# Optimization experiments

Hardware: AMD Instinct MI355X
Metric: run time of the kernel (lower is better)

Reference implementation:

```python
import jax, jax.numpy as jnp
import numpy as np

EPS = 1e-7  # keras.backend.epsilon()
B, U, F = 1024, 256, 31
D = 1 + U + F  # features dim after concat


def setup_inputs() -> dict:
    key = jax.random.key(0)
    ks = jax.random.split(key, 9)
    s = 1.0 / np.sqrt(D)
    return {
        "last_cell": jax.random.uniform(ks[0], (B, U), dtype=jnp.float32),
        "input_precipitation": jax.random.uniform(ks[1], (B,), dtype=jnp.float32),
        "input_other_features": jax.random.normal(ks[2], (B, F), dtype=jnp.float32),
        "W_i": jax.random.normal(ks[3], (D, U), dtype=jnp.float32) * s,
        "b_i": jnp.zeros((U,), dtype=jnp.float32),
        "W_r": jax.random.normal(ks[4], (D, U * U), dtype=jnp.float32) * s,
        "b_r": jnp.zeros((U * U,), dtype=jnp.float32),
        "W_o": jax.random.normal(ks[5], (D, U), dtype=jnp.float32) * s,
        "b_o": jnp.zeros((U,), dtype=jnp.float32),
    }


def reference(last_cell, input_precipitation, input_other_features,
              W_i, b_i, W_r, b_r, W_o, b_o):
    # L1-normalize last cell state (mass fractions)
    l1 = jnp.sum(jnp.abs(last_cell), axis=-1, keepdims=True) + EPS
    last_cell_hat = last_cell / l1
    p = input_precipitation[:, None]  # [B,1]
    features = jnp.concatenate([p, last_cell_hat, input_other_features], axis=-1)  # [B,D]

    # input gate: sigmoid then L1-normalized across units (mass-conserving split)
    ig = jax.nn.sigmoid(features @ W_i + b_i)
    ig = ig / jnp.sum(jnp.abs(ig), axis=-1, keepdims=True)

    # redistribution matrix: relu, reshape [B,U,U], L1-normalize each row
    R = jax.nn.relu(features @ W_r + b_r).reshape(-1, U, U)
    R = R / jnp.sum(jnp.abs(R), axis=-1, keepdims=True)

    # output gate: sigmoid
    og = jax.nn.sigmoid(features @ W_o + b_o)

    cell_in = ig * p                                   # [B,U]
    cell_sys = jnp.einsum('bu,buv->bv', last_cell, R)  # batched (1xU)@(UxU)
    candidate = cell_in + cell_sys
    output = og * candidate
    cell = (1.0 - og) * candidate
    return (cell, output)
```

## Files before the change

### kernel.cpp

```cpp
#include <hip/hip_runtime.h>


#define EPS_L1 1e-7f

constexpr int BB  = 1024;
constexpr int U   = 256;
constexpr int F   = 31;
constexpr int D   = 1 + U + F;
constexpr int NBV = BB * U;
constexpr int NCH = D / 32;
constexpr int UIMGB = NCH * 16384;
constexpr size_t WTB_BYTES  = (size_t)258 * UIMGB;
constexpr size_t FEAT_BYTES = (size_t)BB * D * 2;
constexpr int PITCH = 260;

typedef float f32x4 __attribute__((ext_vector_type(4)));
typedef short bf16x8 __attribute__((ext_vector_type(8)));

__device__ __forceinline__ unsigned f2bf(float x) {
  union { float f; unsigned u; } v; v.f = x;
  unsigned r = v.u + 0x7FFFu + ((v.u >> 16) & 1u);
  return r >> 16;
}

#define GLDS16(gp, lp)                                                        \
  __builtin_amdgcn_global_load_lds(                                          \
      (const __attribute__((address_space(1))) void*)(gp),                   \
      (__attribute__((address_space(3))) void*)(lp), 16, 0, 0)

#define MFMA16(a, b, c) __builtin_amdgcn_mfma_f32_16x16x32_bf16((a), (b), (c), 0, 0, 0)

__global__ __launch_bounds__(256) void k_prepW(
    const float* __restrict__ Wi, const float* __restrict__ Wr,
    const float* __restrict__ Wo, short* __restrict__ WtB) {
  __shared__ short lds[2][32 * PITCH];
  const int bid = blockIdx.x, t = threadIdx.x;
  const int u = bid / 3, part = bid % 3;
  const float* src; long ld;
  if (u < 256)       { src = Wr + (size_t)u * 256; ld = 65536; }
  else if (u == 256) { src = Wi; ld = 256; }
  else               { src = Wo; ld = 256; }
  short* dst = WtB + (size_t)u * 73728;
  const int lane = t & 63, wave = t >> 6;
  const int g = lane >> 4, l15 = lane & 15;

#pragma unroll
  for (int cc = 0; cc < 3; ++cc) {
    const int c = part * 3 + cc;
    short* buf = lds[cc & 1];
#pragma unroll
    for (int i = 0; i < 8; ++i) {
      const int f = i * 256 + t;
      const int row = f >> 6, col4 = f & 63;
      const float4 v = *(const float4*)(src + (size_t)(c * 32 + row) * ld + col4 * 4);
      const unsigned lo = f2bf(v.x) | (f2bf(v.y) << 16);
      const unsigned hi = f2bf(v.z) | (f2bf(v.w) << 16);
      unsigned* wp = (unsigned*)&buf[row * PITCH + col4 * 4];
      wp[0] = lo; wp[1] = hi;
    }
    __syncthreads();
#pragma unroll
    for (int i = 0; i < 4; ++i) {
      const int n0 = wave * 4 + i;
      bf16x8 h;
#pragma unroll
      for (int j = 0; j < 8; ++j)
        h[j] = buf[(g * 8 + j) * PITCH + n0 * 16 + l15];
      *(bf16x8*)(dst + (size_t)(c * 16 + n0) * 512 + lane * 8) = h;
    }
    __syncthreads();
  }
}

__global__ __launch_bounds__(256) void k_prepF(
    const float* __restrict__ lc, const float* __restrict__ p,
    const float* __restrict__ other, short* __restrict__ featImg,
    float* __restrict__ cell_sys) {
  __shared__ float inv_s[64];
  const int bid = blockIdx.x, t = threadIdx.x;
  if (bid < 16) {
    const int b0 = bid * 64;
    const int row = t >> 2, q = t & 3;
    const float4* lp = (const float4*)(lc + (size_t)(b0 + row) * 256 + q * 64);
    float s = 0.f;
#pragma unroll
    for (int j = 0; j < 16; ++j) {
      const float4 v = lp[j];
      s += fabsf(v.x) + fabsf(v.y) + fabsf(v.z) + fabsf(v.w);
    }
    s += __shfl_xor(s, 1, 64);
    s += __shfl_xor(s, 2, 64);
    if (q == 0) inv_s[row] = 1.f / (s + EPS_L1);
    __syncthreads();
#pragma unroll
    for (int i = 0; i < 9; ++i) {
      const int idx = i * 256 + t;
      const int reg = idx >> 6, l = idx & 63;
      const int c = reg >> 2, mt = reg & 3;
      const int lrow = mt * 16 + (l & 15);
      const int grow = b0 + lrow;
      const int k0 = c * 32 + (l >> 4) * 8;
      bf16x8 h;
#pragma unroll
      for (int j = 0; j < 8; ++j) {
        const int k = k0 + j;
        float v;
        if (k == 0) v = p[grow];
        else if (k <= 256) v = lc[(size_t)grow * 256 + (k - 1)] * inv_s[lrow];
        else v = other[(size_t)grow * 31 + (k - 257)];
        h[j] = (short)f2bf(v);
      }
      *(bf16x8*)(featImg + (size_t)bid * 18432 + (size_t)reg * 512 + l * 8) = h;
    }
  } else {
    float4* cs4 = (float4*)cell_sys;
    const int base = (bid - 16) * 8192 + t;
    const float4 z = {0.f, 0.f, 0.f, 0.f};
#pragma unroll
    for (int k2 = 0; k2 < 32; ++k2) cs4[base + k2 * 256] = z;
  }
}

__global__ __launch_bounds__(256, 2) void k_heavyR6(
    const short* __restrict__ featImg, const short* __restrict__ WtB,
    const float* __restrict__ lc, const float* __restrict__ br,
    float* __restrict__ cell_sys) {
  __shared__ short aT[18432];
  __shared__ float rsum[2][64][4];
  __shared__ float lcs[2][64];

  const int t = threadIdx.x, lane = t & 63, cq = t >> 6;
  const int quad = lane >> 4, l15 = lane & 15;
  const int bid = blockIdx.x;
  const int Mb = (bid >> 3) & 15;
  const int ug = (bid & 7) * 4 + (bid >> 7);
  const int b0 = Mb * 64, u0 = ug * 8;

  {
    const char* gA = (const char*)featImg + (size_t)Mb * 36864;
    char* lA = (char*)aT;
#pragma unroll
    for (int i = 0; i < 9; ++i)
      GLDS16(gA + i * 4096 + t * 16, lA + i * 4096 + t * 16);
  }

  const char* aB = (const char*)aT + lane * 16;
  const char* bB = (const char*)WtB + (size_t)u0 * UIMGB + cq * 4096 + lane * 16;

  f32x4 acc[4][4], outa[4][4];
#pragma unroll
  for (int m = 0; m < 4; ++m)
#pragma unroll
    for (int n = 0; n < 4; ++n)
#pragma unroll
      for (int r = 0; r < 4; ++r) { acc[m][n][r] = 0.f; outa[m][n][r] = 0.f; }

  bf16x8 bfr[3][4];
#pragma unroll
  for (int n = 0; n < 4; ++n) bfr[0][n] = *(const bf16x8*)(bB + n * 1024);
#pragma unroll
  for (int n = 0; n < 4; ++n) bfr[1][n] = *(const bf16x8*)(bB + 16384 + n * 1024);

  __syncthreads();

  bf16x8 afr[2][4];
#pragma unroll
  for (int m = 0; m < 4; ++m) afr[0][m] = *(const bf16x8*)(aB + m * 1024);

  for (int uu = 0; uu < 8; ++uu) {
    const int u = u0 + uu;
    float bv[4];
#pragma unroll
    for (int n = 0; n < 4; ++n)
      bv[n] = br[(size_t)u * 256 + cq * 64 + n * 16 + l15];
    if (t < 64) lcs[uu & 1][t] = lc[(size_t)(b0 + t) * 256 + u];

#pragma unroll
    for (int c = 0; c < 9; ++c) {
#pragma unroll
      for (int n = 0; n < 4; ++n)
        bfr[(c + 2) % 3][n] = *(const bf16x8*)(bB + (c + 2) * 16384 + n * 1024);
      if (c < 8) {
#pragma unroll
        for (int m = 0; m < 4; ++m)
          afr[(c + 1) & 1][m] = *(const bf16x8*)(aB + (c + 1) * 4096 + m * 1024);
      }
#pragma unroll
      for (int m = 0; m < 4; ++m)
#pragma unroll
        for (int n = 0; n < 4; ++n)
          acc[m][n] = MFMA16(afr[c & 1][m], bfr[c % 3][n], acc[m][n]);
    }
    bB += UIMGB;

#pragma unroll
    for (int m = 0; m < 4; ++m) afr[0][m] = *(const bf16x8*)(aB + m * 1024);

    const int ub = uu & 1;
    float sm[4][4];
#pragma unroll
    for (int m = 0; m < 4; ++m)
#pragma unroll
      for (int r = 0; r < 4; ++r) {
        float sv = 0.f;
#pragma unroll
        for (int n = 0; n < 4; ++n) {
          const float rv = fmaxf(acc[m][n][r] + bv[n], 0.f);
          acc[m][n][r] = rv;
          sv += rv;
        }
        sm[m][r] = sv;
      }
#pragma unroll
    for (int msk = 1; msk < 16; msk <<= 1)
#pragma unroll
      for (int m = 0; m < 4; ++m)
#pragma unroll
        for (int r = 0; r < 4; ++r)
          sm[m][r] += __shfl_xor(sm[m][r], msk, 64);
    if (l15 == 0) {
#pragma unroll
      for (int m = 0; m < 4; ++m)
#pragma unroll
        for (int r = 0; r < 4; ++r)
          rsum[ub][m * 16 + quad * 4 + r][cq] = sm[m][r];
    }
    __syncthreads();
#pragma unroll
    for (int m = 0; m < 4; ++m)
#pragma unroll
      for (int r = 0; r < 4; ++r) {
        const int row = m * 16 + quad * 4 + r;
        const float4 rv = *(const float4*)&rsum[ub][row][0];
        const float tot = (rv.x + rv.y) + (rv.z + rv.w);
        const float alpha = lcs[ub][row] * __builtin_amdgcn_rcpf(tot);
#pragma unroll
        for (int n = 0; n < 4; ++n) {
          outa[m][n][r] = fmaf(alpha, acc[m][n][r], outa[m][n][r]);
          acc[m][n][r] = 0.f;
        }
      }
  }

#pragma unroll
  for (int m = 0; m < 4; ++m)
#pragma unroll
    for (int r = 0; r < 4; ++r) {
      const int grow = b0 + m * 16 + quad * 4 + r;
#pragma unroll
      for (int n = 0; n < 4; ++n)
        atomicAdd(&cell_sys[(size_t)grow * 256 + cq * 64 + n * 16 + l15],
                  outa[m][n][r]);
    }
}

__global__ __launch_bounds__(512, 2) void k_post(
    const short* __restrict__ featImg, const short* __restrict__ WtB,
    const float* __restrict__ bi, const float* __restrict__ bo,
    const float* __restrict__ p, const float* __restrict__ cell_sys,
    float* __restrict__ dout) {
  __shared__ short aT[18432];
  __shared__ float rsum[64][12];
  __shared__ float ps[64];

  const int t = threadIdx.x, lane = t & 63, cg = t >> 6;
  const int quad = lane >> 4, l15 = lane & 15;
  const int mb = blockIdx.x, b0 = mb * 64;

  {
    const char* gsrc = (const char*)featImg + (size_t)mb * 36864;
    char* lbase = (char*)aT;
#pragma unroll
    for (int i = 0; i < 5; ++i) {
      if (i * 8 + cg < 36) {
        const int off = i * 8192 + t * 16;
        GLDS16(gsrc + off, lbase + off);
      }
    }
  }
  if (t < 64) ps[t] = p[b0 + t];

  f32x4 acc[4][2];
#pragma unroll
  for (int mt = 0; mt < 4; ++mt)
#pragma unroll
    for (int n = 0; n < 2; ++n)
#pragma unroll
      for (int r = 0; r < 4; ++r) acc[mt][n][r] = 0.f;

  const char* bptr = (const char*)WtB + (size_t)256 * UIMGB + cg * 2048 + lane * 16;
  bf16x8 cb0 = *(const bf16x8*)(bptr);
  bf16x8 cb1 = *(const bf16x8*)(bptr + 1024);
  bf16x8 nb0 = *(const bf16x8*)(bptr + 16384);
  bf16x8 nb1 = *(const bf16x8*)(bptr + 16384 + 1024);
  bptr += 32768;

  __syncthreads();

  float ig0[4][4], ig1[4][4], og0[4][4], og1[4][4];

#pragma unroll
  for (int g = 0; g < 2; ++g) {
    const float* bias = (g == 0) ? bi : bo;
    const float bv0 = bias[cg * 32 + l15];
    const float bv1 = bias[cg * 32 + 16 + l15];
#pragma unroll
    for (int c = 0; c < 9; ++c) {
      const bf16x8 pb0 = *(const bf16x8*)(bptr);
      const bf16x8 pb1 = *(const bf16x8*)(bptr + 1024);
      bptr += 16384;
      const char* ab = (const char*)aT + c * 4096 + lane * 16;
      const bf16x8 a0 = *(const bf16x8*)(ab);
      const bf16x8 a1 = *(const bf16x8*)(ab + 1024);
      const bf16x8 a2 = *(const bf16x8*)(ab + 2048);
      const bf16x8 a3 = *(const bf16x8*)(ab + 3072);
      acc[0][0] = MFMA16(a0, cb0, acc[0][0]);
      acc[0][1] = MFMA16(a0, cb1, acc[0][1]);
      acc[1][0] = MFMA16(a1, cb0, acc[1][0]);
      acc[1][1] = MFMA16(a1, cb1, acc[1][1]);
      acc[2][0] = MFMA16(a2, cb0, acc[2][0]);
      acc[2][1] = MFMA16(a2, cb1, acc[2][1]);
      acc[3][0] = MFMA16(a3, cb0, acc[3][0]);
      acc[3][1] = MFMA16(a3, cb1, acc[3][1]);
      cb0 = nb0; cb1 = nb1; nb0 = pb0; nb1 = pb1;
    }

#pragma unroll
    for (int mt = 0; mt < 4; ++mt)
#pragma unroll
      for (int r = 0; r < 4; ++r) {
        const float v0 = 1.f / (1.f + __expf(-(acc[mt][0][r] + bv0)));
        const float v1 = 1.f / (1.f + __expf(-(acc[mt][1][r] + bv1)));
        if (g == 0) { ig0[mt][r] = v0; ig1[mt][r] = v1; }
        else        { og0[mt][r] = v0; og1[mt][r] = v1; }
        acc[mt][0][r] = 0.f;
        acc[mt][1][r] = 0.f;
      }

    if (g == 0) {
      float sm[4][4];
#pragma unroll
      for (int mt = 0; mt < 4; ++mt)
#pragma unroll
        for (int r = 0; r < 4; ++r) sm[mt][r] = ig0[mt][r] + ig1[mt][r];
#pragma unroll
      for (int msk = 1; msk < 16; msk <<= 1)
#pragma unroll
        for (int mt = 0; mt < 4; ++mt)
#pragma unroll
          for (int r = 0; r < 4; ++r)
            sm[mt][r] += __shfl_xor(sm[mt][r], msk, 64);
      if (l15 == 0) {
#pragma unroll
        for (int mt = 0; mt < 4; ++mt)
#pragma unroll
          for (int r = 0; r < 4; ++r)
            rsum[mt * 16 + quad * 4 + r][cg] = sm[mt][r];
      }
      __syncthreads();
#pragma unroll
      for (int mt = 0; mt < 4; ++mt)
#pragma unroll
        for (int r = 0; r < 4; ++r) {
          const int row = mt * 16 + quad * 4 + r;
          const float4 ra = *(const float4*)&rsum[row][0];
          const float4 rb = *(const float4*)&rsum[row][4];
          const float inv = 1.f / (((ra.x + ra.y) + (ra.z + ra.w)) +
                                   ((rb.x + rb.y) + (rb.z + rb.w)));
          ig0[mt][r] *= inv;
          ig1[mt][r] *= inv;
        }
    }
  }

#pragma unroll
  for (int mt = 0; mt < 4; ++mt)
#pragma unroll
    for (int r = 0; r < 4; ++r) {
      const int row = mt * 16 + quad * 4 + r;
      const float pr = ps[row];
      const size_t base = (size_t)(b0 + row) * 256 + cg * 32 + l15;
      {
        const float cand = fmaf(ig0[mt][r], pr, cell_sys[base]);
        dout[base] = (1.f - og0[mt][r]) * cand;
        dout[NBV + base] = og0[mt][r] * cand;
      }
      {
        const float cand = fmaf(ig1[mt][r], pr, cell_sys[base + 16]);
        dout[base + 16] = (1.f - og1[mt][r]) * cand;
        dout[NBV + base + 16] = og1[mt][r] * cand;
      }
    }
}

extern "C" void kernel_launch(void* const* d_in, const int* in_sizes, int n_in,
                              void* d_out, int out_size, void* d_ws, size_t ws_size,
                              hipStream_t stream) {
  const float* lc    = (const float*)d_in[0];
  const float* p     = (const float*)d_in[1];
  const float* other = (const float*)d_in[2];
  const float* Wi    = (const float*)d_in[3];
  const float* bi    = (const float*)d_in[4];
  const float* Wr    = (const float*)d_in[5];
  const float* br    = (const float*)d_in[6];
  const float* Wo    = (const float*)d_in[7];
  const float* bo    = (const float*)d_in[8];
  float* out = (float*)d_out;

  char* wsb = (char*)d_ws;
  short* WtB      = (short*)wsb;
  short* featImg  = (short*)(wsb + WTB_BYTES);
  float* cell_sys = (float*)(wsb + WTB_BYTES + FEAT_BYTES);

  k_prepW<<<774, 256, 0, stream>>>(Wi, Wr, Wo, WtB);
  k_prepF<<<24, 256, 0, stream>>>(lc, p, other, featImg, cell_sys);
  k_heavyR6<<<512, 256, 0, stream>>>(featImg, WtB, lc, br, cell_sys);
  k_post<<<16, 512, 0, stream>>>(featImg, WtB, bi, bo, p, cell_sys, out);
}
```

Baseline: 222.8 us.

## Switch to 32x32 MFMA, fold gate GEMMs into heavy kernel, add final elementwise pass

Re-lays out the bf16 weight and feature images for 32x32x16 MFMA tiles and rewrites the heavy redistribution kernel to use them, halving accumulator tile count and cross-lane reduction width changes. The input/output gate GEMMs move from the separate k_post kernel into 16 extra blocks of the heavy kernel that write ig and og to the output buffer, and a new small elementwise kernel combines them with cell_sys. This aims to cut MFMA instruction count and remove the serialized low-occupancy post kernel, at the cost of an extra global round trip for ig/og and an additional launch.

```diff
diff --git a/kernel.cpp b/kernel.cpp
--- a/kernel.cpp
+++ b/kernel.cpp
@@ -14,7 +14,7 @@
 constexpr size_t FEAT_BYTES = (size_t)BB * D * 2;
 constexpr int PITCH = 260;
 
-typedef float f32x4 __attribute__((ext_vector_type(4)));
+typedef float f32x16 __attribute__((ext_vector_type(16)));
 typedef short bf16x8 __attribute__((ext_vector_type(8)));
 
 __device__ __forceinline__ unsigned f2bf(float x) {
@@ -28,7 +28,7 @@
       (const __attribute__((address_space(1))) void*)(gp),                   \
       (__attribute__((address_space(3))) void*)(lp), 16, 0, 0)
 
-#define MFMA16(a, b, c) __builtin_amdgcn_mfma_f32_16x16x32_bf16((a), (b), (c), 0, 0, 0)
+#define MFMA32(a, b, c) __builtin_amdgcn_mfma_f32_32x32x16_bf16((a), (b), (c), 0, 0, 0)
 
 __global__ __launch_bounds__(256) void k_prepW(
     const float* __restrict__ Wi, const float* __restrict__ Wr,
@@ -42,7 +42,7 @@
   else               { src = Wo; ld = 256; }
   short* dst = WtB + (size_t)u * 73728;
   const int lane = t & 63, wave = t >> 6;
-  const int g = lane >> 4, l15 = lane & 15;
+  const int g2 = lane >> 5, l31 = lane & 31;
 
 #pragma unroll
   for (int cc = 0; cc < 3; ++cc) {
@@ -62,11 +62,12 @@
 #pragma unroll
     for (int i = 0; i < 4; ++i) {
       const int n0 = wave * 4 + i;
-      bf16x8 h;
+      const int nt = n0 >> 1, h = n0 & 1;
+      bf16x8 hv;
 #pragma unroll
       for (int j = 0; j < 8; ++j)
-        h[j] = buf[(g * 8 + j) * PITCH + n0 * 16 + l15];
-      *(bf16x8*)(dst + (size_t)(c * 16 + n0) * 512 + lane * 8) = h;
+        hv[j] = buf[(h * 16 + g2 * 8 + j) * PITCH + nt * 32 + l31];
+      *(bf16x8*)(dst + (size_t)(c * 16 + n0) * 512 + lane * 8) = hv;
     }
     __syncthreads();
   }
@@ -96,11 +97,12 @@
     for (int i = 0; i < 9; ++i) {
       const int idx = i * 256 + t;
       const int reg = idx >> 6, l = idx & 63;
-      const int c = reg >> 2, mt = reg & 3;
-      const int lrow = mt * 16 + (l & 15);
+      const int c = reg >> 2, sub = reg & 3;
+      const int mt = sub >> 1, h = sub & 1;
+      const int lrow = mt * 32 + (l & 31);
       const int grow = b0 + lrow;
-      const int k0 = c * 32 + (l >> 4) * 8;
-      bf16x8 h;
+      const int k0 = c * 32 + h * 16 + (l >> 5) * 8;
+      bf16x8 hv;
 #pragma unroll
       for (int j = 0; j < 8; ++j) {
         const int k = k0 + j;
@@ -108,9 +110,9 @@
         if (k == 0) v = p[grow];
         else if (k <= 256) v = lc[(size_t)grow * 256 + (k - 1)] * inv_s[lrow];
         else v = other[(size_t)grow * 31 + (k - 257)];
-        h[j] = (short)f2bf(v);
-      }
-      *(bf16x8*)(featImg + (size_t)bid * 18432 + (size_t)reg * 512 + l * 8) = h;
+        hv[j] = (short)f2bf(v);
+      }
+      *(bf16x8*)(featImg + (size_t)bid * 18432 + (size_t)reg * 512 + l * 8) = hv;
     }
   } else {
     float4* cs4 = (float4*)cell_sys;
@@ -121,20 +123,23 @@
   }
 }
 
-__global__ __launch_bounds__(256, 2) void k_heavyR6(
+__global__ __launch_bounds__(256, 2) void k_heavyG(
     const short* __restrict__ featImg, const short* __restrict__ WtB,
     const float* __restrict__ lc, const float* __restrict__ br,
-    float* __restrict__ cell_sys) {
+    const float* __restrict__ bi, const float* __restrict__ bo,
+    float* __restrict__ cell_sys, float* __restrict__ dout) {
   __shared__ short aT[18432];
   __shared__ float rsum[2][64][4];
   __shared__ float lcs[2][64];
 
   const int t = threadIdx.x, lane = t & 63, cq = t >> 6;
-  const int quad = lane >> 4, l15 = lane & 15;
+  const int g2 = lane >> 5, l31 = lane & 31;
   const int bid = blockIdx.x;
-  const int Mb = (bid >> 3) & 15;
-  const int ug = (bid & 7) * 4 + (bid >> 7);
-  const int b0 = Mb * 64, u0 = ug * 8;
+  const bool is_gate = bid >= 512;
+  const int Mb = is_gate ? (bid - 512) : ((bid >> 3) & 15);
+  const int ug = is_gate ? 0 : ((bid & 7) * 4 + (bid >> 7));
+  const int b0 = Mb * 64;
+  const int u0 = ug * 8;
 
   {
     const char* gA = (const char*)featImg + (size_t)Mb * 36864;
@@ -145,252 +150,221 @@
   }
 
   const char* aB = (const char*)aT + lane * 16;
-  const char* bB = (const char*)WtB + (size_t)u0 * UIMGB + cq * 4096 + lane * 16;
-
-  f32x4 acc[4][4], outa[4][4];
-#pragma unroll
-  for (int m = 0; m < 4; ++m)
-#pragma unroll
-    for (int n = 0; n < 4; ++n)
-#pragma unroll
-      for (int r = 0; r < 4; ++r) { acc[m][n][r] = 0.f; outa[m][n][r] = 0.f; }
+  const char* bB = (const char*)WtB +
+      (is_gate ? (size_t)256 * UIMGB : (size_t)u0 * UIMGB) +
+      cq * 4096 + lane * 16;
+
+  f32x16 acc[2][2];
+#pragma unroll
+  for (int m = 0; m < 2; ++m)
+#pragma unroll
+    for (int n = 0; n < 2; ++n)
+#pragma unroll
+      for (int r = 0; r < 16; ++r) acc[m][n][r] = 0.f;
 
   bf16x8 bfr[3][4];
 #pragma unroll
-  for (int n = 0; n < 4; ++n) bfr[0][n] = *(const bf16x8*)(bB + n * 1024);
-#pragma unroll
-  for (int n = 0; n < 4; ++n) bfr[1][n] = *(const bf16x8*)(bB + 16384 + n * 1024);
+  for (int q = 0; q < 4; ++q) bfr[0][q] = *(const bf16x8*)(bB + q * 1024);
+#pragma unroll
+  for (int q = 0; q < 4; ++q) bfr[1][q] = *(const bf16x8*)(bB + 16384 + q * 1024);
 
   __syncthreads();
 
   bf16x8 afr[2][4];
 #pragma unroll
-  for (int m = 0; m < 4; ++m) afr[0][m] = *(const bf16x8*)(aB + m * 1024);
-
-  for (int uu = 0; uu < 8; ++uu) {
-    const int u = u0 + uu;
-    float bv[4];
-#pragma unroll
-    for (int n = 0; n < 4; ++n)
-      bv[n] = br[(size_t)u * 256 + cq * 64 + n * 16 + l15];
-    if (t < 64) lcs[uu & 1][t] = lc[(size_t)(b0 + t) * 256 + u];
-
-#pragma unroll
-    for (int c = 0; c < 9; ++c) {
-#pragma unroll
-      for (int n = 0; n < 4; ++n)
-        bfr[(c + 2) % 3][n] = *(const bf16x8*)(bB + (c + 2) * 16384 + n * 1024);
-      if (c < 8) {
-#pragma unroll
-        for (int m = 0; m < 4; ++m)
-          afr[(c + 1) & 1][m] = *(const bf16x8*)(aB + (c + 1) * 4096 + m * 1024);
-      }
-#pragma unroll
-      for (int m = 0; m < 4; ++m)
-#pragma unroll
-        for (int n = 0; n < 4; ++n)
-          acc[m][n] = MFMA16(afr[c & 1][m], bfr[c % 3][n], acc[m][n]);
-    }
-    bB += UIMGB;
-
-#pragma unroll
-    for (int m = 0; m < 4; ++m) afr[0][m] = *(const bf16x8*)(aB + m * 1024);
-
-    const int ub = uu & 1;
-    float sm[4][4];
-#pragma unroll
-    for (int m = 0; m < 4; ++m)
-#pragma unroll
-      for (int r = 0; r < 4; ++r) {
-        float sv = 0.f;
-#pragma unroll
-        for (int n = 0; n < 4; ++n) {
-          const float rv = fmaxf(acc[m][n][r] + bv[n], 0.f);
-          acc[m][n][r] = rv;
-          sv += rv;
-        }
-        sm[m][r] = sv;
-      }
-#pragma unroll
-    for (int msk = 1; msk < 16; msk <<= 1)
-#pragma unroll
-      for (int m = 0; m < 4; ++m)
-#pragma unroll
-        for (int r = 0; r < 4; ++r)
-          sm[m][r] += __shfl_xor(sm[m][r], msk, 64);
-    if (l15 == 0) {
-#pragma unroll
-      for (int m = 0; m < 4; ++m)
-#pragma unroll
-        for (int r = 0; r < 4; ++r)
-          rsum[ub][m * 16 + quad * 4 + r][cq] = sm[m][r];
-    }
-    __syncthreads();
-#pragma unroll
-    for (int m = 0; m < 4; ++m)
-#pragma unroll
-      for (int r = 0; r < 4; ++r) {
-        const int row = m * 16 + quad * 4 + r;
-        const float4 rv = *(const float4*)&rsum[ub][row][0];
-        const float tot = (rv.x + rv.y) + (rv.z + rv.w);
-        const float alpha = lcs[ub][row] * __builtin_amdgcn_rcpf(tot);
-#pragma unroll
-        for (int n = 0; n < 4; ++n) {
-          outa[m][n][r] = fmaf(alpha, acc[m][n][r], outa[m][n][r]);
-          acc[m][n][r] = 0.f;
-        }
-      }
+  for (int q = 0; q < 4; ++q) afr[0][q] = *(const bf16x8*)(aB + q * 1024);
+
+  if (!is_gate) {
+    f32x16 outa[2][2];
+#pragma unroll
+    for (int m = 0; m < 2; ++m)
+#pragma unroll
+      for (int n = 0; n < 2; ++n)
+#pragma unroll
+        for (int r = 0; r < 16; ++r) outa[m][n][r] = 0.f;
+
+    for (int uu = 0; uu < 8; ++uu) {
+      const int u = u0 + uu;
+      float bv[2];
+#pragma unroll
+      for (int n = 0; n < 2; ++n)
+        bv[n] = br[(size_t)u * 256 + cq * 64 + n * 32 + l31];
+      if (t < 64) lcs[uu & 1][t] = lc[(size_t)(b0 + t) * 256 + u];
+
+#pragma unroll
+      for (int c = 0; c < 9; ++c) {
+#pragma unroll
+        for (int q = 0; q < 4; ++q)
+          bfr[(c + 2) % 3][q] = *(const bf16x8*)(bB + (c + 2) * 16384 + q * 1024);
+        if (c < 8) {
+#pragma unroll
+          for (int q = 0; q < 4; ++q)
+            afr[(c + 1) & 1][q] = *(const bf16x8*)(aB + (c + 1) * 4096 + q * 1024);
+        }
+        const int as = c & 1, bs = c % 3;
+#pragma unroll
+        for (int m = 0; m < 2; ++m)
+#pragma unroll
+          for (int n = 0; n < 2; ++n) {
+            acc[m][n] = MFMA32(afr[as][m * 2],     bfr[bs][n * 2],     acc[m][n]);
+            acc[m][n] = MFMA32(afr[as][m * 2 + 1], bfr[bs][n * 2 + 1], acc[m][n]);
+          }
+      }
+      bB += UIMGB;
+#pragma unroll
+      for (int q = 0; q < 4; ++q) afr[0][q] = *(const bf16x8*)(aB + q * 1024);
+
+      const int ub = uu & 1;
+      float sm[2][16];
+#pragma unroll
+      for (int m = 0; m < 2; ++m)
+#pragma unroll
+        for (int r = 0; r < 16; ++r) {
+          const float r0v = fmaxf(acc[m][0][r] + bv[0], 0.f);
+          const float r1v = fmaxf(acc[m][1][r] + bv[1], 0.f);
+          acc[m][0][r] = r0v; acc[m][1][r] = r1v;
+          sm[m][r] = r0v + r1v;
+        }
+#pragma unroll
+      for (int msk = 1; msk < 32; msk <<= 1)
+#pragma unroll
+        for (int m = 0; m < 2; ++m)
+#pragma unroll
+          for (int r = 0; r < 16; ++r)
+            sm[m][r] += __shfl_xor(sm[m][r], msk, 64);
+      if (l31 == 0) {
+#pragma unroll
+        for (int m = 0; m < 2; ++m)
+#pragma unroll
+          for (int r = 0; r < 16; ++r)
+            rsum[ub][m * 32 + (r & 3) + 8 * (r >> 2) + 4 * g2][cq] = sm[m][r];
+      }
+      __syncthreads();
+#pragma unroll
+      for (int m = 0; m < 2; ++m)
+#pragma unroll
+        for (int r = 0; r < 16; ++r) {
+          const int row = m * 32 + (r & 3) + 8 * (r >> 2) + 4 * g2;
+          const float4 rv = *(const float4*)&rsum[ub][row][0];
+          const float tot = (rv.x + rv.y) + (rv.z + rv.w);
+          const float alpha = lcs[ub][row] * __builtin_amdgcn_rcpf(tot);
+          outa[m][0][r] = fmaf(alpha, acc[m][0][r], outa[m][0][r]);
+          outa[m][1][r] = fmaf(alpha, acc[m][1][r], outa[m][1][r]);
+          acc[m][0][r] = 0.f;
+          acc[m][1][r] = 0.f;
+        }
+    }
+
+#pragma unroll
+    for (int m = 0; m < 2; ++m)
+#pragma unroll
+      for (int r = 0; r < 16; ++r) {
+        const int grow = b0 + m * 32 + (r & 3) + 8 * (r >> 2) + 4 * g2;
+#pragma unroll
+        for (int n = 0; n < 2; ++n)
+          atomicAdd(&cell_sys[(size_t)grow * 256 + cq * 64 + n * 32 + l31],
+                    outa[m][n][r]);
+      }
+  } else {
+#pragma unroll
+    for (int g = 0; g < 2; ++g) {
+      const float* bias = (g == 0) ? bi : bo;
+      float bv[2];
+#pragma unroll
+      for (int n = 0; n < 2; ++n) bv[n] = bias[cq * 64 + n * 32 + l31];
+
+#pragma unroll
+      for (int c = 0; c < 9; ++c) {
+#pragma unroll
+        for (int q = 0; q < 4; ++q)
+          bfr[(c + 2) % 3][q] = *(const bf16x8*)(bB + (c + 2) * 16384 + q * 1024);
+        if (c < 8) {
+#pragma unroll
+          for (int q = 0; q < 4; ++q)
+            afr[(c + 1) & 1][q] = *(const bf16x8*)(aB + (c + 1) * 4096 + q * 1024);
+        }
+        const int as = c & 1, bs = c % 3;
+#pragma unroll
+        for (int m = 0; m < 2; ++m)
+#pragma unroll
+          for (int n = 0; n < 2; ++n) {
+            acc[m][n] = MFMA32(afr[as][m * 2],     bfr[bs][n * 2],     acc[m][n]);
+            acc[m][n] = MFMA32(afr[as][m * 2 + 1], bfr[bs][n * 2 + 1], acc[m][n]);
+          }
+      }
+      bB += UIMGB;
+#pragma unroll
+      for (int q = 0; q < 4; ++q) afr[0][q] = *(const bf16x8*)(aB + q * 1024);
+
+#pragma unroll
+      for (int m = 0; m < 2; ++m)
+#pragma unroll
+        for (int n = 0; n < 2; ++n)
+#pragma unroll
+          for (int r = 0; r < 16; ++r)
+            acc[m][n][r] = 1.f / (1.f + __expf(-(acc[m][n][r] + bv[n])));
+
+      if (g == 0) {
+        float sm[2][16];
+#pragma unroll
+        for (int m = 0; m < 2; ++m)
+#pragma unroll
+          for (int r = 0; r < 16; ++r) sm[m][r] = acc[m][0][r] + acc[m][1][r];
+#pragma unroll
+        for (int msk = 1; msk < 32; msk <<= 1)
+#pragma unroll
+          for (int m = 0; m < 2; ++m)
+#pragma unroll
+            for (int r = 0; r < 16; ++r)
+              sm[m][r] += __shfl_xor(sm[m][r], msk, 64);
+        if (l31 == 0) {
+#pragma unroll
+          for (int m = 0; m < 2; ++m)
+#pragma unroll
+            for (int r = 0; r < 16; ++r)
+              rsum[0][m * 32 + (r & 3) + 8 * (r >> 2) + 4 * g2][cq] = sm[m][r];
+        }
+        __syncthreads();
+#pragma unroll
+        for (int m = 0; m < 2; ++m)
+#pragma unroll
+          for (int r = 0; r < 16; ++r) {
+            const int row = m * 32 + (r & 3) + 8 * (r >> 2) + 4 * g2;
+            const float4 rv = *(const float4*)&rsum[0][row][0];
+            const float inv = 1.f / ((rv.x + rv.y) + (rv.z + rv.w));
+#pragma unroll
+            for (int n = 0; n < 2; ++n) {
+              dout[(size_t)(b0 + row) * 256 + cq * 64 + n * 32 + l31] =
+                  acc[m][n][r] * inv;
+              acc[m][n][r] = 0.f;
+            }
+          }
+      } else {
+#pragma unroll
+        for (int m = 0; m < 2; ++m)
+#pragma unroll
+          for (int r = 0; r < 16; ++r) {
+            const int row = m * 32 + (r & 3) + 8 * (r >> 2) + 4 * g2;
+#pragma unroll
+            for (int n = 0; n < 2; ++n)
+              dout[(size_t)NBV + (size_t)(b0 + row) * 256 + cq * 64 + n * 32 + l31] =
+                  acc[m][n][r];
+          }
+      }
+    }
   }
-
-#pragma unroll
-  for (int m = 0; m < 4; ++m)
-#pragma unroll
-    for (int r = 0; r < 4; ++r) {
-      const int grow = b0 + m * 16 + quad * 4 + r;
-#pragma unroll
-      for (int n = 0; n < 4; ++n)
-        atomicAdd(&cell_sys[(size_t)grow * 256 + cq * 64 + n * 16 + l15],
-                  outa[m][n][r]);
-    }
-}
-
-__global__ __launch_bounds__(512, 2) void k_post(
-    const short* __restrict__ featImg, const short* __restrict__ WtB,
-    const float* __restrict__ bi, const float* __restrict__ bo,
-    const float* __restrict__ p, const float* __restrict__ cell_sys,
-    float* __restrict__ dout) {
-  __shared__ short aT[18432];
-  __shared__ float rsum[64][12];
-  __shared__ float ps[64];
-
-  const int t = threadIdx.x, lane = t & 63, cg = t >> 6;
-  const int quad = lane >> 4, l15 = lane & 15;
-  const int mb = blockIdx.x, b0 = mb * 64;
-
-  {
-    const char* gsrc = (const char*)featImg + (size_t)mb * 36864;
-    char* lbase = (char*)aT;
-#pragma unroll
-    for (int i = 0; i < 5; ++i) {
-      if (i * 8 + cg < 36) {
-        const int off = i * 8192 + t * 16;
-        GLDS16(gsrc + off, lbase + off);
-      }
-    }
-  }
-  if (t < 64) ps[t] = p[b0 + t];
-
-  f32x4 acc[4][2];
-#pragma unroll
-  for (int mt = 0; mt < 4; ++mt)
-#pragma unroll
-    for (int n = 0; n < 2; ++n)
-#pragma unroll
-      for (int r = 0; r < 4; ++r) acc[mt][n][r] = 0.f;
-
-  const char* bptr = (const char*)WtB + (size_t)256 * UIMGB + cg * 2048 + lane * 16;
-  bf16x8 cb0 = *(const bf16x8*)(bptr);
-  bf16x8 cb1 = *(const bf16x8*)(bptr + 1024);
-  bf16x8 nb0 = *(const bf16x8*)(bptr + 16384);
-  bf16x8 nb1 = *(const bf16x8*)(bptr + 16384 + 1024);
-  bptr += 32768;
-
-  __syncthreads();
-
-  float ig0[4][4], ig1[4][4], og0[4][4], og1[4][4];
-
-#pragma unroll
-  for (int g = 0; g < 2; ++g) {
-    const float* bias = (g == 0) ? bi : bo;
-    const float bv0 = bias[cg * 32 + l15];
-    const float bv1 = bias[cg * 32 + 16 + l15];
-#pragma unroll
-    for (int c = 0; c < 9; ++c) {
-      const bf16x8 pb0 = *(const bf16x8*)(bptr);
-      const bf16x8 pb1 = *(const bf16x8*)(bptr + 1024);
-      bptr += 16384;
-      const char* ab = (const char*)aT + c * 4096 + lane * 16;
-      const bf16x8 a0 = *(const bf16x8*)(ab);
-      const bf16x8 a1 = *(const bf16x8*)(ab + 1024);
-      const bf16x8 a2 = *(const bf16x8*)(ab + 2048);
-      const bf16x8 a3 = *(const bf16x8*)(ab + 3072);
-      acc[0][0] = MFMA16(a0, cb0, acc[0][0]);
-      acc[0][1] = MFMA16(a0, cb1, acc[0][1]);
-      acc[1][0] = MFMA16(a1, cb0, acc[1][0]);
-      acc[1][1] = MFMA16(a1, cb1, acc[1][1]);
-      acc[2][0] = MFMA16(a2, cb0, acc[2][0]);
-      acc[2][1] = MFMA16(a2, cb1, acc[2][1]);
-      acc[3][0] = MFMA16(a3, cb0, acc[3][0]);
-      acc[3][1] = MFMA16(a3, cb1, acc[3][1]);
-      cb0 = nb0; cb1 = nb1; nb0 = pb0; nb1 = pb1;
-    }
-
-#pragma unroll
-    for (int mt = 0; mt < 4; ++mt)
-#pragma unroll
-      for (int r = 0; r < 4; ++r) {
-        const float v0 = 1.f / (1.f + __expf(-(acc[mt][0][r] + bv0)));
-        const float v1 = 1.f / (1.f + __expf(-(acc[mt][1][r] + bv1)));
-        if (g == 0) { ig0[mt][r] = v0; ig1[mt][r] = v1; }
-        else        { og0[mt][r] = v0; og1[mt][r] = v1; }
-        acc[mt][0][r] = 0.f;
-        acc[mt][1][r] = 0.f;
-      }
-
-    if (g == 0) {
-      float sm[4][4];
-#pragma unroll
-      for (int mt = 0; mt < 4; ++mt)
-#pragma unroll
-        for (int r = 0; r < 4; ++r) sm[mt][r] = ig0[mt][r] + ig1[mt][r];
-#pragma unroll
-      for (int msk = 1; msk < 16; msk <<= 1)
-#pragma unroll
-        for (int mt = 0; mt < 4; ++mt)
-#pragma unroll
-          for (int r = 0; r < 4; ++r)
-            sm[mt][r] += __shfl_xor(sm[mt][r], msk, 64);
-      if (l15 == 0) {
-#pragma unroll
-        for (int mt = 0; mt < 4; ++mt)
-#pragma unroll
-          for (int r = 0; r < 4; ++r)
-            rsum[mt * 16 + quad * 4 + r][cg] = sm[mt][r];
-      }
-      __syncthreads();
-#pragma unroll
-      for (int mt = 0; mt < 4; ++mt)
-#pragma unroll
-        for (int r = 0; r < 4; ++r) {
-          const int row = mt * 16 + quad * 4 + r;
-          const float4 ra = *(const float4*)&rsum[row][0];
-          const float4 rb = *(const float4*)&rsum[row][4];
-          const float inv = 1.f / (((ra.x + ra.y) + (ra.z + ra.w)) +
-                                   ((rb.x + rb.y) + (rb.z + rb.w)));
-          ig0[mt][r] *= inv;
-          ig1[mt][r] *= inv;
-        }
-    }
-  }
-
-#pragma unroll
-  for (int mt = 0; mt < 4; ++mt)
-#pragma unroll
-    for (int r = 0; r < 4; ++r) {
-      const int row = mt * 16 + quad * 4 + r;
-      const float pr = ps[row];
-      const size_t base = (size_t)(b0 + row) * 256 + cg * 32 + l15;
-      {
-        const float cand = fmaf(ig0[mt][r], pr, cell_sys[base]);
-        dout[base] = (1.f - og0[mt][r]) * cand;
-        dout[NBV + base] = og0[mt][r] * cand;
-      }
-      {
-        const float cand = fmaf(ig1[mt][r], pr, cell_sys[base + 16]);
-        dout[base + 16] = (1.f - og1[mt][r]) * cand;
-        dout[NBV + base + 16] = og1[mt][r] * cand;
-      }
-    }
+}
+
+__global__ __launch_bounds__(256) void k_final(
+    const float* __restrict__ cell_sys, const float* __restrict__ p,
+    float* __restrict__ d_out) {
+  const int i = blockIdx.x * 256 + threadIdx.x;
+  const float ig = d_out[i];
+  const float ogv = d_out[NBV + i];
+  const float cand = fmaf(ig, p[i >> 8], cell_sys[i]);
+  const float outp = ogv * cand;
+  d_out[i] = (1.0f - ogv) * cand;
+  d_out[NBV + i] = outp;
 }
 
 extern "C" void kernel_launch(void* const* d_in, const int* in_sizes, int n_in,
@@ -414,6 +388,6 @@
 
   k_prepW<<<774, 256, 0, stream>>>(Wi, Wr, Wo, WtB);
   k_prepF<<<24, 256, 0, stream>>>(lc, p, other, featImg, cell_sys);
-  k_heavyR6<<<512, 256, 0, stream>>>(featImg, WtB, lc, br, cell_sys);
-  k_post<<<16, 512, 0, stream>>>(featImg, WtB, bi, bo, p, cell_sys, out);
-}
+  k_heavyG<<<528, 256, 0, stream>>>(featImg, WtB, lc, br, bi, bo, cell_sys, out);
+  k_final<<<1024, 256, 0, stream>>>(cell_sys, p, out);
+}
```

After: 241.3 us. 8.3% more time.
